# Kernel tuning notes

Hardware: AMD Instinct MI355X
Metric: run time of the kernel (lower is better)

## Reference

```python
import jax, jax.numpy as jnp
import numpy as np

CHANNEL = 1
ALPHA = 1.0
EPS = 1e-10
SHAPE = (1, CHANNEL, 160, 192, 160)


def _sobel_kernels(channel):
    s2 = np.array([[-1., 0., 1.], [-2., 0., 2.], [-1., 0., 1.]], dtype=np.float32)
    # sobel.repeat(channel,1,3,1,1): 2D kernel tiled along depth -> k[d,h,w] = s2[h,w]
    kx = np.tile(s2[None, :, :], (3, 1, 1))
    ky = np.tile(s2.T[None, :, :], (3, 1, 1))
    kz = np.array([[[-1., -1., -1.], [-2., -2., -2.], [-1., -1., -1.]],
                   [[0., 0., 0.], [0., 0., 0.], [0., 0., 0.]],
                   [[1., 1., 1.], [2., 2., 2.], [1., 1., 1.]]], dtype=np.float32)
    def rep(k):  # -> [channel, 1, 3, 3, 3] for depthwise conv
        return jnp.asarray(np.tile(k[None, None], (channel, 1, 1, 1, 1)))
    return rep(kx), rep(ky), rep(kz)


def _conv3d(x, k, channel):
    # torch F.conv3d (cross-correlation), padding=1, groups=channel
    return jax.lax.conv_general_dilated(
        x, k, window_strides=(1, 1, 1), padding=((1, 1), (1, 1), (1, 1)),
        dimension_numbers=('NCDHW', 'OIDHW', 'NCDHW'),
        feature_group_count=channel)


def setup_inputs() -> dict:
    key = jax.random.key(0)
    k1, k2, k3 = jax.random.split(key, 3)
    M = jax.random.normal(k1, SHAPE, dtype=jnp.float32)
    S = jax.random.normal(k2, SHAPE, dtype=jnp.float32)
    flow = jax.random.normal(k3, (SHAPE[0], 3) + SHAPE[2:], dtype=jnp.float32)
    return {"M": M, "S": S, "flow": flow}


def reference(M, S, flow):
    kx, ky, kz = _sobel_kernels(CHANNEL)
    Idiff = M - S
    Sx = _conv3d(S, kx, CHANNEL)
    Sy = _conv3d(S, ky, CHANNEL)
    Sz = _conv3d(S, kz, CHANNEL)
    Mx = _conv3d(M, kx, CHANNEL)
    My = _conv3d(M, ky, CHANNEL)
    Mz = _conv3d(M, kz, CHANNEL)
    Sxyz_mag = Sx ** 2 + Sy ** 2 + Sz ** 2
    Mxyz_mag = Mx ** 2 + My ** 2 + Mz ** 2
    denom_S = Sxyz_mag + (ALPHA ** 2) * Idiff ** 2 + 1e-10
    denom_M = Mxyz_mag + (ALPHA ** 2) * Idiff ** 2 + 1e-10
    Ux = Idiff * (Sx / denom_S + Mx / denom_M)
    Uy = Idiff * (Sy / denom_S + My / denom_M)
    Uz = Idiff * (Sz / denom_S + Mz / denom_M)
    demons_ori_xz = jnp.arctan(Ux / (Uz + EPS))
    demons_ori_yz = jnp.arctan(Uy / (Uz + EPS))
    flow_ori_xz = jnp.arctan(flow[:, 0] / (flow[:, 2] + EPS))
    flow_ori_yz = jnp.arctan(flow[:, 1] / (flow[:, 2] + EPS))
    ori_error = jnp.mean((flow_ori_xz - demons_ori_xz) ** 2) + \
                jnp.mean((flow_ori_yz - demons_ori_yz) ** 2)
    return ori_error
```

## Files before the change

### kernel.cpp

```cpp
#include <hip/hip_runtime.h>
#include <math.h>

#define DD 160
#define HH 192
#define WW 160
#define TW 32
#define THB 16
#define TD 8
#define HW (HH * WW)
#define NVOX (DD * HW)
#define HTW 34
#define HTH 18
#define LSTR 34
#define HALO (HTH * HTW)

typedef float v2f __attribute__((ext_vector_type(2)));

__device__ __forceinline__ v2f vrcp(v2f a) {
    v2f r;
    r.x = __builtin_amdgcn_rcpf(a.x);
    r.y = __builtin_amdgcn_rcpf(a.y);
    return r;
}

__device__ __forceinline__ v2f atanv(v2f r) {
    v2f ar = __builtin_elementwise_abs(r);
    v2f inv = vrcp(ar);
    v2f x = __builtin_elementwise_min(ar, inv);
    v2f x2 = x * x;
    v2f p = __builtin_elementwise_fma(x2,
            __builtin_elementwise_fma(x2,
            __builtin_elementwise_fma(x2,
            __builtin_elementwise_fma(x2,
            __builtin_elementwise_fma(x2, (v2f)(-0.0117212f), (v2f)(0.05265332f)),
            (v2f)(-0.11643287f)), (v2f)(0.19354346f)), (v2f)(-0.33262347f)),
            (v2f)(0.99997726f));
    p *= x;
    v2f q = 1.57079632679489662f - p;
    v2f res;
    res.x = ar.x > 1.0f ? q.x : p.x;
    res.y = ar.y > 1.0f ? q.y : p.y;
    res.x = copysignf(res.x, r.x);
    res.y = copysignf(res.y, r.y);
    return res;
}

__global__ __launch_bounds__(256) void demons_ori_kernel(
    const float* __restrict__ Mv, const float* __restrict__ Sv,
    const float* __restrict__ flow, float* __restrict__ out)
{
    __shared__ float buf[2][2][HTH * LSTR];
    __shared__ float redbuf[4];

    const int tid = threadIdx.x;
    const int lane = tid & 63;
    const int wid = tid >> 6;
    const int tw = lane & 31;
    const int r  = wid * 4 + (lane >> 5) * 2;
    const int w0 = blockIdx.x * TW;
    const int h0 = blockIdx.y * THB;
    const int d0 = blockIdx.z * TD;

    const bool has2 = (tid < HALO - 512);
    int gb0, gb1, gb2 = 0;
    bool ok0, ok1, ok2 = false;
    {
        int i = tid;
        int hh = i / HTW, ww = i - HTW * hh;
        int gh = h0 + hh - 1, gw = w0 + ww - 1;
        ok0 = (gh >= 0 && gh < HH && gw >= 0 && gw < WW);
        gb0 = gh * WW + gw;
        i = tid + 256;
        hh = i / HTW; ww = i - HTW * hh;
        gh = h0 + hh - 1; gw = w0 + ww - 1;
        ok1 = (gh >= 0 && gh < HH && gw >= 0 && gw < WW);
        gb1 = gh * WW + gw;
        if (has2) {
            i = tid + 512;
            hh = i / HTW; ww = i - HTW * hh;
            gh = h0 + hh - 1; gw = w0 + ww - 1;
            ok2 = (gh >= 0 && gh < HH && gw >= 0 && gw < WW);
            gb2 = gh * WW + gw;
        }
    }

    float pS0 = 0.f, pM0 = 0.f, pS1 = 0.f, pM1 = 0.f, pS2 = 0.f, pM2 = 0.f;

    auto issue = [&](int d) {
        const bool din = (d >= 0) && (d < DD);
        const size_t base = (size_t)d * HW;
        pS0 = (din && ok0) ? Sv[base + gb0] : 0.f;
        pM0 = (din && ok0) ? Mv[base + gb0] : 0.f;
        pS1 = (din && ok1) ? Sv[base + gb1] : 0.f;
        pM1 = (din && ok1) ? Mv[base + gb1] : 0.f;
        pS2 = (din && ok2) ? Sv[base + gb2] : 0.f;
        pM2 = (din && ok2) ? Mv[base + gb2] : 0.f;
    };
    auto commit = [&](int d) {
        float* __restrict__ bS = &buf[d & 1][0][0];
        float* __restrict__ bM = &buf[d & 1][1][0];
        bS[tid] = pS0;        bM[tid] = pM0;
        bS[tid + 256] = pS1;  bM[tid + 256] = pM1;
        if (has2) { bS[tid + 512] = pS2; bM[tid + 512] = pM2; }
    };

    const int rb = r * LSTR + tw;
    auto fieldPartials = [&](const float* __restrict__ b,
                             v2f& Px, v2f& Py, v2f& Bq, v2f& Cq) {
        const float* r0 = b + rb;
        const float* r1 = r0 + LSTR;
        const float* r2 = r1 + LSTR;
        const float* r3 = r2 + LSTR;
        float a0 = r0[0], b0 = r0[1], c0 = r0[2];
        float a1 = r1[0], b1 = r1[1], c1 = r1[2];
        float a2 = r2[0], b2 = r2[1], c2 = r2[2];
        float a3 = r3[0], b3 = r3[1], c3 = r3[2];
        float X0 = c0 - a0, X1 = c1 - a1, X2 = c2 - a2, X3 = c3 - a3;
        float W0 = a0 + 2.f * b0 + c0, W1 = a1 + 2.f * b1 + c1;
        float W2 = a2 + 2.f * b2 + c2, W3 = a3 + 2.f * b3 + c3;
        float I0 = a0 + b0 + c0, I1 = a1 + b1 + c1;
        float I2 = a2 + b2 + c2, I3 = a3 + b3 + c3;
        Px = (v2f){X0 + 2.f * X1 + X2, X1 + 2.f * X2 + X3};
        Py = (v2f){W2 - W0, W3 - W1};
        Bq = (v2f){I0 + 2.f * I1 + I2, I1 + 2.f * I2 + I3};
        Cq = (v2f){b1, b2};
    };

    v2f mSPx, mSPy, mSB, mSC, mMPx, mMPy, mMB, mMC;
    v2f zSPx, zSPy, zSB, zSC, zMPx, zMPy, zMB, zMC;
    v2f pSPx, pSPy, pSB, pSC, pMPx, pMPy, pMB, pMC;

    issue(d0 - 1);
    commit(d0 - 1);
    issue(d0);
    __syncthreads();
    fieldPartials(&buf[(d0 - 1) & 1][0][0], mSPx, mSPy, mSB, mSC);
    fieldPartials(&buf[(d0 - 1) & 1][1][0], mMPx, mMPy, mMB, mMC);
    commit(d0);
    issue(d0 + 1);
    __syncthreads();
    fieldPartials(&buf[d0 & 1][0][0], zSPx, zSPy, zSB, zSC);
    fieldPartials(&buf[d0 & 1][1][0], zMPx, zMPy, zMB, zMC);

    const size_t voffA = (size_t)(h0 + r) * WW + (w0 + tw);
    v2f fFx, fFy, fFz;
    {
        size_t o = (size_t)d0 * HW + voffA;
        fFx = (v2f){flow[o], flow[o + WW]};
        fFy = (v2f){flow[NVOX + o], flow[NVOX + o + WW]};
        fFz = (v2f){flow[2 * (size_t)NVOX + o], flow[2 * (size_t)NVOX + o + WW]};
    }

    v2f vsum = (v2f){0.f, 0.f};

    #pragma unroll
    for (int dd = 0; dd < TD; ++dd) {
        const int d = d0 + dd;
        commit(d + 1);
        v2f nFx = (v2f){0.f, 0.f}, nFy = nFx, nFz = nFx;
        if (dd < TD - 1) {
            issue(d + 2);
            size_t o = (size_t)(d + 1) * HW + voffA;
            nFx = (v2f){flow[o], flow[o + WW]};
            nFy = (v2f){flow[NVOX + o], flow[NVOX + o + WW]};
            nFz = (v2f){flow[2 * (size_t)NVOX + o], flow[2 * (size_t)NVOX + o + WW]};
        }
        __syncthreads();
        fieldPartials(&buf[(d + 1) & 1][0][0], pSPx, pSPy, pSB, pSC);
        fieldPartials(&buf[(d + 1) & 1][1][0], pMPx, pMPy, pMB, pMC);

        v2f idf = zMC - zSC;
        v2f i2  = __builtin_elementwise_fma(idf, idf, (v2f)(1e-10f));
        v2f gxS = mSPx + zSPx + pSPx;
        v2f gyS = mSPy + zSPy + pSPy;
        v2f gzS = pSB - mSB;
        v2f gxM = mMPx + zMPx + pMPx;
        v2f gyM = mMPy + zMPy + pMPy;
        v2f gzM = pMB - mMB;
        v2f denS = __builtin_elementwise_fma(gxS, gxS,
                   __builtin_elementwise_fma(gyS, gyS,
                   __builtin_elementwise_fma(gzS, gzS, i2)));
        v2f denM = __builtin_elementwise_fma(gxM, gxM,
                   __builtin_elementwise_fma(gyM, gyM,
                   __builtin_elementwise_fma(gzM, gzM, i2)));
        v2f rS = vrcp(denS);
        v2f rM = vrcp(denM);
        v2f Ux = idf * __builtin_elementwise_fma(gxS, rS, gxM * rM);
        v2f Uy = idf * __builtin_elementwise_fma(gyS, rS, gyM * rM);
        v2f Uz = idf * __builtin_elementwise_fma(gzS, rS, gzM * rM);
        v2f rz = vrcp(Uz + 1e-10f);
        v2f dxz = atanv(Ux * rz);
        v2f dyz = atanv(Uy * rz);

        v2f rf = vrcp(fFz + 1e-10f);
        v2f fxz = atanv(fFx * rf);
        v2f fyz = atanv(fFy * rf);

        v2f e1 = fxz - dxz;
        v2f e2 = fyz - dyz;
        vsum = __builtin_elementwise_fma(e1, e1,
               __builtin_elementwise_fma(e2, e2, vsum));

        mSPx = zSPx; mSPy = zSPy; mSB = zSB; mSC = zSC;
        mMPx = zMPx; mMPy = zMPy; mMB = zMB; mMC = zMC;
        zSPx = pSPx; zSPy = pSPy; zSB = pSB; zSC = pSC;
        zMPx = pMPx; zMPy = pMPy; zMB = pMB; zMC = pMC;
        fFx = nFx; fFy = nFy; fFz = nFz;
    }

    float lsum = vsum.x + vsum.y;
    #pragma unroll
    for (int o = 32; o > 0; o >>= 1)
        lsum += __shfl_down(lsum, o, 64);
    if (lane == 0)
        redbuf[wid] = lsum;
    __syncthreads();
    if (tid == 0) {
        float s = redbuf[0] + redbuf[1] + redbuf[2] + redbuf[3];
        atomicAdd(out, s * (1.0f / (float)NVOX));
    }
}

extern "C" void kernel_launch(void* const* d_in, const int* in_sizes, int n_in,
                              void* d_out, int out_size, void* d_ws, size_t ws_size,
                              hipStream_t stream) {
    const float* Mv   = (const float*)d_in[0];
    const float* Sv   = (const float*)d_in[1];
    const float* flow = (const float*)d_in[2];
    float* out = (float*)d_out;

    hipMemsetAsync(out, 0, sizeof(float), stream);

    dim3 grid(WW / TW, HH / THB, DD / TD);
    demons_ori_kernel<<<grid, dim3(256), 0, stream>>>(Mv, Sv, flow, out);
}
```

Measured before the change: 129.1 us.

## Give each wavefront a private halo tile to drop block-wide barriers

Each of the four wavefronts now owns a 16x8 sub-tile with its own 18x10 halo in a private LDS double buffer, so the per-slice __syncthreads are removed and the waves rely on in-wave ordering. The cost being targeted is barrier stalls across the 256-thread block. In exchange, the halo overhead per output voxel grows, since the smaller tiles mean more redundant global loads, and the unroll is reduced to 2. Correctness depends on the implicit lockstep of each wavefront on LDS writes followed by reads with no barrier.

```diff
diff --git a/kernel.cpp b/kernel.cpp
--- a/kernel.cpp
+++ b/kernel.cpp
@@ -4,15 +4,18 @@
 #define DD 160
 #define HH 192
 #define WW 160
-#define TW 32
-#define THB 16
+#define WTW 16
+#define WTH 8
+#define BWX 32
+#define BWY 16
 #define TD 8
 #define HW (HH * WW)
 #define NVOX (DD * HW)
-#define HTW 34
-#define HTH 18
-#define LSTR 34
+#define HTW 18
+#define HTH 10
+#define LSTR 24
 #define HALO (HTH * HTW)
+#define WBUF (HTH * LSTR)
 
 typedef float v2f __attribute__((ext_vector_type(2)));
 
@@ -49,36 +52,39 @@
     const float* __restrict__ Mv, const float* __restrict__ Sv,
     const float* __restrict__ flow, float* __restrict__ out)
 {
-    __shared__ float buf[2][2][HTH * LSTR];
+    __shared__ float buf[4][2][2][WBUF];
     __shared__ float redbuf[4];
 
     const int tid = threadIdx.x;
+    const int wid = tid >> 6;
     const int lane = tid & 63;
-    const int wid = tid >> 6;
-    const int tw = lane & 31;
-    const int r  = wid * 4 + (lane >> 5) * 2;
-    const int w0 = blockIdx.x * TW;
-    const int h0 = blockIdx.y * THB;
+    const int tw = lane & 15;
+    const int r  = (lane >> 4) * 2;
+    const int w0 = blockIdx.x * BWX + (wid & 1) * WTW;
+    const int h0 = blockIdx.y * BWY + (wid >> 1) * WTH;
     const int d0 = blockIdx.z * TD;
 
-    const bool has2 = (tid < HALO - 512);
-    int gb0, gb1, gb2 = 0;
+    const bool has2 = (lane < HALO - 128);
+    int idx0, idx1, idx2 = 0, gb0, gb1, gb2 = 0;
     bool ok0, ok1, ok2 = false;
     {
-        int i = tid;
+        int i = lane;
         int hh = i / HTW, ww = i - HTW * hh;
         int gh = h0 + hh - 1, gw = w0 + ww - 1;
+        idx0 = hh * LSTR + ww;
         ok0 = (gh >= 0 && gh < HH && gw >= 0 && gw < WW);
         gb0 = gh * WW + gw;
-        i = tid + 256;
+        i = lane + 64;
         hh = i / HTW; ww = i - HTW * hh;
         gh = h0 + hh - 1; gw = w0 + ww - 1;
+        idx1 = hh * LSTR + ww;
         ok1 = (gh >= 0 && gh < HH && gw >= 0 && gw < WW);
         gb1 = gh * WW + gw;
         if (has2) {
-            i = tid + 512;
+            i = lane + 128;
             hh = i / HTW; ww = i - HTW * hh;
             gh = h0 + hh - 1; gw = w0 + ww - 1;
+            idx2 = hh * LSTR + ww;
             ok2 = (gh >= 0 && gh < HH && gw >= 0 && gw < WW);
             gb2 = gh * WW + gw;
         }
@@ -97,11 +103,11 @@
         pM2 = (din && ok2) ? Mv[base + gb2] : 0.f;
     };
     auto commit = [&](int d) {
-        float* __restrict__ bS = &buf[d & 1][0][0];
-        float* __restrict__ bM = &buf[d & 1][1][0];
-        bS[tid] = pS0;        bM[tid] = pM0;
-        bS[tid + 256] = pS1;  bM[tid + 256] = pM1;
-        if (has2) { bS[tid + 512] = pS2; bM[tid + 512] = pM2; }
+        float* __restrict__ bS = &buf[wid][d & 1][0][0];
+        float* __restrict__ bM = &buf[wid][d & 1][1][0];
+        bS[idx0] = pS0;  bM[idx0] = pM0;
+        bS[idx1] = pS1;  bM[idx1] = pM1;
+        if (has2) { bS[idx2] = pS2; bM[idx2] = pM2; }
     };
 
     const int rb = r * LSTR + tw;
@@ -133,14 +139,12 @@
     issue(d0 - 1);
     commit(d0 - 1);
     issue(d0);
-    __syncthreads();
-    fieldPartials(&buf[(d0 - 1) & 1][0][0], mSPx, mSPy, mSB, mSC);
-    fieldPartials(&buf[(d0 - 1) & 1][1][0], mMPx, mMPy, mMB, mMC);
+    fieldPartials(&buf[wid][(d0 - 1) & 1][0][0], mSPx, mSPy, mSB, mSC);
+    fieldPartials(&buf[wid][(d0 - 1) & 1][1][0], mMPx, mMPy, mMB, mMC);
     commit(d0);
     issue(d0 + 1);
-    __syncthreads();
-    fieldPartials(&buf[d0 & 1][0][0], zSPx, zSPy, zSB, zSC);
-    fieldPartials(&buf[d0 & 1][1][0], zMPx, zMPy, zMB, zMC);
+    fieldPartials(&buf[wid][d0 & 1][0][0], zSPx, zSPy, zSB, zSC);
+    fieldPartials(&buf[wid][d0 & 1][1][0], zMPx, zMPy, zMB, zMC);
 
     const size_t voffA = (size_t)(h0 + r) * WW + (w0 + tw);
     v2f fFx, fFy, fFz;
@@ -153,7 +157,7 @@
 
     v2f vsum = (v2f){0.f, 0.f};
 
-    #pragma unroll
+    #pragma unroll 2
     for (int dd = 0; dd < TD; ++dd) {
         const int d = d0 + dd;
         commit(d + 1);
@@ -165,9 +169,8 @@
             nFy = (v2f){flow[NVOX + o], flow[NVOX + o + WW]};
             nFz = (v2f){flow[2 * (size_t)NVOX + o], flow[2 * (size_t)NVOX + o + WW]};
         }
-        __syncthreads();
-        fieldPartials(&buf[(d + 1) & 1][0][0], pSPx, pSPy, pSB, pSC);
-        fieldPartials(&buf[(d + 1) & 1][1][0], pMPx, pMPy, pMB, pMC);
+        fieldPartials(&buf[wid][(d + 1) & 1][0][0], pSPx, pSPy, pSB, pSC);
+        fieldPartials(&buf[wid][(d + 1) & 1][1][0], pMPx, pMPy, pMB, pMC);
 
         v2f idf = zMC - zSC;
         v2f i2  = __builtin_elementwise_fma(idf, idf, (v2f)(1e-10f));
@@ -231,6 +234,6 @@
 
     hipMemsetAsync(out, 0, sizeof(float), stream);
 
-    dim3 grid(WW / TW, HH / THB, DD / TD);
+    dim3 grid(WW / BWX, HH / BWY, DD / TD);
     demons_ori_kernel<<<grid, dim3(256), 0, stream>>>(Mv, Sv, flow, out);
 }
```

After: 134.6 us. 4.2% more time.

## Replace LDS halo staging with direct global stencil loads and clamped masks

Applied to the files above, without the earlier changes.

Drops the double-buffered shared-memory halo tiles and their per-slice __syncthreads. Each thread now reads its 4x3 stencil neighbourhood directly from global memory, clamping indices and multiplying by 0/1 masks to reproduce the zero padding. The software prefetch of the next slice and of the flow values is removed, and the depth loop is only partially unrolled. This relies on L1/L2 caching for neighbour reuse and issues many more global load instructions per voxel, with less latency hiding.

```diff
diff --git a/kernel.cpp b/kernel.cpp
--- a/kernel.cpp
+++ b/kernel.cpp
@@ -4,15 +4,9 @@
 #define DD 160
 #define HH 192
 #define WW 160
-#define TW 32
-#define THB 16
 #define TD 8
 #define HW (HH * WW)
 #define NVOX (DD * HW)
-#define HTW 34
-#define HTH 18
-#define LSTR 34
-#define HALO (HTH * HTW)
 
 typedef float v2f __attribute__((ext_vector_type(2)));
 
@@ -49,72 +43,47 @@
     const float* __restrict__ Mv, const float* __restrict__ Sv,
     const float* __restrict__ flow, float* __restrict__ out)
 {
-    __shared__ float buf[2][2][HTH * LSTR];
     __shared__ float redbuf[4];
 
     const int tid = threadIdx.x;
+    const int wid = tid >> 6;
     const int lane = tid & 63;
-    const int wid = tid >> 6;
     const int tw = lane & 31;
-    const int r  = wid * 4 + (lane >> 5) * 2;
-    const int w0 = blockIdx.x * TW;
-    const int h0 = blockIdx.y * THB;
+    const int g  = lane >> 5;
+    const int w0 = blockIdx.x * 32;
+    const int h0 = blockIdx.y * 16;
     const int d0 = blockIdx.z * TD;
+    const int c  = w0 + tw;
+    const int rb = h0 + wid * 4 + g * 2;
 
-    const bool has2 = (tid < HALO - 512);
-    int gb0, gb1, gb2 = 0;
-    bool ok0, ok1, ok2 = false;
-    {
-        int i = tid;
-        int hh = i / HTW, ww = i - HTW * hh;
-        int gh = h0 + hh - 1, gw = w0 + ww - 1;
-        ok0 = (gh >= 0 && gh < HH && gw >= 0 && gw < WW);
-        gb0 = gh * WW + gw;
-        i = tid + 256;
-        hh = i / HTW; ww = i - HTW * hh;
-        gh = h0 + hh - 1; gw = w0 + ww - 1;
-        ok1 = (gh >= 0 && gh < HH && gw >= 0 && gw < WW);
-        gb1 = gh * WW + gw;
-        if (has2) {
-            i = tid + 512;
-            hh = i / HTW; ww = i - HTW * hh;
-            gh = h0 + hh - 1; gw = w0 + ww - 1;
-            ok2 = (gh >= 0 && gh < HH && gw >= 0 && gw < WW);
-            gb2 = gh * WW + gw;
-        }
-    }
+    const int cm = (c > 0) ? c - 1 : 0;
+    const int cp = (c < WW - 1) ? c + 1 : WW - 1;
+    const float fm = (c > 0) ? 1.f : 0.f;
+    const float fp = (c < WW - 1) ? 1.f : 0.f;
 
-    float pS0 = 0.f, pM0 = 0.f, pS1 = 0.f, pM1 = 0.f, pS2 = 0.f, pM2 = 0.f;
+    int gh0 = rb - 1, gh1 = rb, gh2 = rb + 1, gh3 = rb + 2;
+    const float f0 = (gh0 >= 0 && gh0 < HH) ? 1.f : 0.f;
+    const float f1 = 1.f;
+    const float f2 = 1.f;
+    const float f3 = (gh3 < HH) ? 1.f : 0.f;
+    gh0 = (gh0 < 0) ? 0 : gh0;
+    gh3 = (gh3 >= HH) ? HH - 1 : gh3;
 
-    auto issue = [&](int d) {
-        const bool din = (d >= 0) && (d < DD);
-        const size_t base = (size_t)d * HW;
-        pS0 = (din && ok0) ? Sv[base + gb0] : 0.f;
-        pM0 = (din && ok0) ? Mv[base + gb0] : 0.f;
-        pS1 = (din && ok1) ? Sv[base + gb1] : 0.f;
-        pM1 = (din && ok1) ? Mv[base + gb1] : 0.f;
-        pS2 = (din && ok2) ? Sv[base + gb2] : 0.f;
-        pM2 = (din && ok2) ? Mv[base + gb2] : 0.f;
-    };
-    auto commit = [&](int d) {
-        float* __restrict__ bS = &buf[d & 1][0][0];
-        float* __restrict__ bM = &buf[d & 1][1][0];
-        bS[tid] = pS0;        bM[tid] = pM0;
-        bS[tid + 256] = pS1;  bM[tid + 256] = pM1;
-        if (has2) { bS[tid + 512] = pS2; bM[tid + 512] = pM2; }
-    };
+    const int o0m = gh0 * WW + cm, o00 = gh0 * WW + c, o0p = gh0 * WW + cp;
+    const int o1m = gh1 * WW + cm, o10 = gh1 * WW + c, o1p = gh1 * WW + cp;
+    const int o2m = gh2 * WW + cm, o20 = gh2 * WW + c, o2p = gh2 * WW + cp;
+    const int o3m = gh3 * WW + cm, o30 = gh3 * WW + c, o3p = gh3 * WW + cp;
+    const float k0m = f0 * fm, k00 = f0, k0p = f0 * fp;
+    const float k1m = f1 * fm, k10 = f1, k1p = f1 * fp;
+    const float k2m = f2 * fm, k20 = f2, k2p = f2 * fp;
+    const float k3m = f3 * fm, k30 = f3, k3p = f3 * fp;
 
-    const int rb = r * LSTR + tw;
-    auto fieldPartials = [&](const float* __restrict__ b,
+    auto fieldPartials = [&](const float* __restrict__ p,
                              v2f& Px, v2f& Py, v2f& Bq, v2f& Cq) {
-        const float* r0 = b + rb;
-        const float* r1 = r0 + LSTR;
-        const float* r2 = r1 + LSTR;
-        const float* r3 = r2 + LSTR;
-        float a0 = r0[0], b0 = r0[1], c0 = r0[2];
-        float a1 = r1[0], b1 = r1[1], c1 = r1[2];
-        float a2 = r2[0], b2 = r2[1], c2 = r2[2];
-        float a3 = r3[0], b3 = r3[1], c3 = r3[2];
+        float a0 = p[o0m] * k0m, b0 = p[o00] * k00, c0 = p[o0p] * k0p;
+        float a1 = p[o1m] * k1m, b1 = p[o10] * k10, c1 = p[o1p] * k1p;
+        float a2 = p[o2m] * k2m, b2 = p[o20] * k20, c2 = p[o2p] * k2p;
+        float a3 = p[o3m] * k3m, b3 = p[o30] * k30, c3 = p[o3p] * k3p;
         float X0 = c0 - a0, X1 = c1 - a1, X2 = c2 - a2, X3 = c3 - a3;
         float W0 = a0 + 2.f * b0 + c0, W1 = a1 + 2.f * b1 + c1;
         float W2 = a2 + 2.f * b2 + c2, W3 = a3 + 2.f * b3 + c3;
@@ -126,48 +95,40 @@
         Cq = (v2f){b1, b2};
     };
 
+    auto computeSlice = [&](int s,
+                            v2f& SPx, v2f& SPy, v2f& SB, v2f& SC,
+                            v2f& MPx, v2f& MPy, v2f& MB, v2f& MC) {
+        if (s >= 0 && s < DD) {
+            const float* pS = Sv + (size_t)s * HW;
+            const float* pM = Mv + (size_t)s * HW;
+            fieldPartials(pS, SPx, SPy, SB, SC);
+            fieldPartials(pM, MPx, MPy, MB, MC);
+        } else {
+            SPx = SPy = SB = SC = (v2f){0.f, 0.f};
+            MPx = MPy = MB = MC = (v2f){0.f, 0.f};
+        }
+    };
+
     v2f mSPx, mSPy, mSB, mSC, mMPx, mMPy, mMB, mMC;
     v2f zSPx, zSPy, zSB, zSC, zMPx, zMPy, zMB, zMC;
     v2f pSPx, pSPy, pSB, pSC, pMPx, pMPy, pMB, pMC;
 
-    issue(d0 - 1);
-    commit(d0 - 1);
-    issue(d0);
-    __syncthreads();
-    fieldPartials(&buf[(d0 - 1) & 1][0][0], mSPx, mSPy, mSB, mSC);
-    fieldPartials(&buf[(d0 - 1) & 1][1][0], mMPx, mMPy, mMB, mMC);
-    commit(d0);
-    issue(d0 + 1);
-    __syncthreads();
-    fieldPartials(&buf[d0 & 1][0][0], zSPx, zSPy, zSB, zSC);
-    fieldPartials(&buf[d0 & 1][1][0], zMPx, zMPy, zMB, zMC);
+    computeSlice(d0 - 1, mSPx, mSPy, mSB, mSC, mMPx, mMPy, mMB, mMC);
+    computeSlice(d0,     zSPx, zSPy, zSB, zSC, zMPx, zMPy, zMB, zMC);
 
-    const size_t voffA = (size_t)(h0 + r) * WW + (w0 + tw);
-    v2f fFx, fFy, fFz;
-    {
-        size_t o = (size_t)d0 * HW + voffA;
-        fFx = (v2f){flow[o], flow[o + WW]};
-        fFy = (v2f){flow[NVOX + o], flow[NVOX + o + WW]};
-        fFz = (v2f){flow[2 * (size_t)NVOX + o], flow[2 * (size_t)NVOX + o + WW]};
-    }
+    const size_t voffA = (size_t)rb * WW + c;
 
     v2f vsum = (v2f){0.f, 0.f};
 
-    #pragma unroll
+    #pragma unroll 2
     for (int dd = 0; dd < TD; ++dd) {
         const int d = d0 + dd;
-        commit(d + 1);
-        v2f nFx = (v2f){0.f, 0.f}, nFy = nFx, nFz = nFx;
-        if (dd < TD - 1) {
-            issue(d + 2);
-            size_t o = (size_t)(d + 1) * HW + voffA;
-            nFx = (v2f){flow[o], flow[o + WW]};
-            nFy = (v2f){flow[NVOX + o], flow[NVOX + o + WW]};
-            nFz = (v2f){flow[2 * (size_t)NVOX + o], flow[2 * (size_t)NVOX + o + WW]};
-        }
-        __syncthreads();
-        fieldPartials(&buf[(d + 1) & 1][0][0], pSPx, pSPy, pSB, pSC);
-        fieldPartials(&buf[(d + 1) & 1][1][0], pMPx, pMPy, pMB, pMC);
+        computeSlice(d + 1, pSPx, pSPy, pSB, pSC, pMPx, pMPy, pMB, pMC);
+
+        size_t o = (size_t)d * HW + voffA;
+        v2f fFx = (v2f){flow[o], flow[o + WW]};
+        v2f fFy = (v2f){flow[NVOX + o], flow[NVOX + o + WW]};
+        v2f fFz = (v2f){flow[2 * (size_t)NVOX + o], flow[2 * (size_t)NVOX + o + WW]};
 
         v2f idf = zMC - zSC;
         v2f i2  = __builtin_elementwise_fma(idf, idf, (v2f)(1e-10f));
@@ -205,7 +166,6 @@
         mMPx = zMPx; mMPy = zMPy; mMB = zMB; mMC = zMC;
         zSPx = pSPx; zSPy = pSPy; zSB = pSB; zSC = pSC;
         zMPx = pMPx; zMPy = pMPy; zMB = pMB; zMC = pMC;
-        fFx = nFx; fFy = nFy; fFz = nFz;
     }
 
     float lsum = vsum.x + vsum.y;
@@ -231,6 +191,6 @@
 
     hipMemsetAsync(out, 0, sizeof(float), stream);
 
-    dim3 grid(WW / TW, HH / THB, DD / TD);
+    dim3 grid(WW / 32, HH / 16, DD / TD);
     demons_ori_kernel<<<grid, dim3(256), 0, stream>>>(Mv, Sv, flow, out);
 }
```

New measurement: 139.1 us. 7.7% more time.
